# Kernel tuning notes

Measured on AMD Instinct MI355X. Metric: run time of the kernel, lower is better.

## Reference

```python
import jax, jax.numpy as jnp
import numpy as np

B, S, D = 8, 2048, 256


def setup_inputs() -> dict:
    key = jax.random.key(0)
    kq, kk, kv, km = jax.random.split(key, 4)
    q = jax.random.normal(kq, (B, S, D), dtype=jnp.float32)
    k = jax.random.normal(kk, (B, S, D), dtype=jnp.float32)
    v = jax.random.normal(kv, (B, S, D), dtype=jnp.float32)
    mask = jax.random.randint(km, (B, S, S), 0, 2, dtype=jnp.int32)
    return {"q": q, "k": k, "v": v, "mask": mask}


def reference(q, k, v, mask):
    d_k = q.shape[-1]
    scale = 1.0 / jnp.sqrt(jnp.float32(d_k))
    # scores: [B, S, S]
    attn = jnp.einsum('bqd,bkd->bqk', q, k) * scale
    attn = jnp.where(mask == 0, jnp.float32(-1e9), attn)
    attn = jax.nn.softmax(attn, axis=-1)
    out = jnp.einsum('bqk,bkd->bqd', attn, v)
    return (out, attn)
```

## Files before the change

kernel.cpp:

```cpp
#include <hip/hip_runtime.h>

constexpr int B = 8, S = 2048, D = 256;
constexpr int TQ = 32;
constexpr float SCALE = 0.0625f;
constexpr int PSTRIDE = 2056;

typedef __attribute__((ext_vector_type(8))) short bf16x8;
typedef __attribute__((ext_vector_type(4))) float f32x4;

__device__ __forceinline__ short f2bf(float f) {
    union { float f; unsigned u; } c; c.f = f;
    unsigned u = c.u + 0x7fffu + ((c.u >> 16) & 1u);
    return (short)(u >> 16);
}

__global__ __launch_bounds__(256) void prepass(
    const float* __restrict__ k, const float* __restrict__ v,
    short* __restrict__ kb, short* __restrict__ vtb)
{
    __shared__ float tile[64][65];
    const int blk = blockIdx.x;
    const int tid = threadIdx.x;

    if (blk < 4096) {
        int i = blk * 256 + tid;
        float4 x = ((const float4*)k)[i];
        short4 o; o.x = f2bf(x.x); o.y = f2bf(x.y); o.z = f2bf(x.z); o.w = f2bf(x.w);
        ((short4*)kb)[i] = o;
    } else {
        int blk2 = blk - 4096;
        int b = blk2 >> 7, rem = blk2 & 127;
        int d0 = (rem & 3) * 64, k0 = (rem >> 2) * 64;
        int tr = tid >> 4, tc = tid & 15;
        const float* vb = v + (size_t)b * S * D;
        #pragma unroll
        for (int r = 0; r < 4; ++r) {
            int key = r * 16 + tr;
            float4 x = *(const float4*)(vb + (size_t)(k0 + key) * D + d0 + tc * 4);
            tile[key][tc * 4 + 0] = x.x; tile[key][tc * 4 + 1] = x.y;
            tile[key][tc * 4 + 2] = x.z; tile[key][tc * 4 + 3] = x.w;
        }
        __syncthreads();
        short* vtbb = vtb + (size_t)b * D * S;
        #pragma unroll
        for (int r = 0; r < 4; ++r) {
            int d = r * 16 + tr;
            short4 o;
            o.x = f2bf(tile[tc * 4 + 0][d]); o.y = f2bf(tile[tc * 4 + 1][d]);
            o.z = f2bf(tile[tc * 4 + 2][d]); o.w = f2bf(tile[tc * 4 + 3][d]);
            *(short4*)(vtbb + (size_t)(d0 + d) * S + k0 + tc * 4) = o;
        }
    }
}

__global__ __launch_bounds__(512, 2) void attn_mfma(
    const float* __restrict__ qf, const short* __restrict__ kb,
    const short* __restrict__ vtb, const int* __restrict__ maskg,
    float* __restrict__ outg, float* __restrict__ attng)
{
    const int b = blockIdx.x & 7;
    const int i0 = (blockIdx.x >> 3) * TQ;
    const int tid = threadIdx.x;
    const int wave = tid >> 6, lane = tid & 63;
    const int quad = lane >> 4, l16 = lane & 15;

    __shared__ short p_lds[TQ][PSTRIDE];
    __shared__ float red[8][TQ];

    unsigned long long mb[2];
    #pragma unroll
    for (int mt = 0; mt < 2; ++mt) {
        const int* mrow = maskg + ((size_t)b * S + i0 + mt * 16 + l16) * S + wave * 256 + quad * 4;
        unsigned long long bits = 0;
        #pragma unroll
        for (int c = 0; c < 2; ++c) {
            int4 t[8];
            #pragma unroll
            for (int j = 0; j < 8; ++j)
                t[j] = *(const int4*)(mrow + (c * 8 + j) * 16);
            #pragma unroll
            for (int j = 0; j < 8; ++j) {
                const int nt = c * 8 + j;
                unsigned long long nib = (t[j].x != 0 ? 1ull : 0ull)
                                       | (t[j].y != 0 ? 2ull : 0ull)
                                       | (t[j].z != 0 ? 4ull : 0ull)
                                       | (t[j].w != 0 ? 8ull : 0ull);
                bits |= nib << (nt * 4);
            }
        }
        mb[mt] = bits;
    }

    bf16x8 aq[2][8];
    const float* qbase = qf + ((size_t)b * S + i0) * D;
    #pragma unroll
    for (int mt = 0; mt < 2; ++mt)
        #pragma unroll
        for (int ks = 0; ks < 8; ++ks) {
            const float* p = qbase + (size_t)(mt * 16 + l16) * D + ks * 32 + quad * 8;
            float4 x0 = *(const float4*)p;
            float4 x1 = *(const float4*)(p + 4);
            bf16x8 a;
            a[0] = f2bf(x0.x); a[1] = f2bf(x0.y); a[2] = f2bf(x0.z); a[3] = f2bf(x0.w);
            a[4] = f2bf(x1.x); a[5] = f2bf(x1.y); a[6] = f2bf(x1.z); a[7] = f2bf(x1.w);
            aq[mt][ks] = a;
        }

    f32x4 acc[2][16];
    #pragma unroll
    for (int mt = 0; mt < 2; ++mt)
        #pragma unroll
        for (int nt = 0; nt < 16; ++nt)
            acc[mt][nt] = f32x4{0.f, 0.f, 0.f, 0.f};

    const short* kbase = kb + (size_t)b * S * D;
    #pragma unroll
    for (int nt = 0; nt < 16; ++nt) {
        const int n0 = wave * 256 + nt * 16;
        bf16x8 bk[8];
        #pragma unroll
        for (int ks = 0; ks < 8; ++ks)
            bk[ks] = *(const bf16x8*)(kbase + (size_t)(n0 + l16) * D + ks * 32 + quad * 8);
        #pragma unroll
        for (int ks = 0; ks < 8; ++ks) {
            acc[0][nt] = __builtin_amdgcn_mfma_f32_16x16x32_bf16(bk[ks], aq[0][ks], acc[0][nt], 0, 0, 0);
            acc[1][nt] = __builtin_amdgcn_mfma_f32_16x16x32_bf16(bk[ks], aq[1][ks], acc[1][nt], 0, 0, 0);
        }
    }

    float rsum[2] = {0.f, 0.f};
    #pragma unroll
    for (int mt = 0; mt < 2; ++mt) {
        #pragma unroll
        for (int nt = 0; nt < 16; ++nt) {
            #pragma unroll
            for (int r = 0; r < 4; ++r) {
                float e = ((mb[mt] >> (nt * 4 + r)) & 1ull)
                        ? __expf(acc[mt][nt][r] * SCALE) : 0.0f;
                acc[mt][nt][r] = e;
                rsum[mt] += e;
            }
        }
    }
    #pragma unroll
    for (int mt = 0; mt < 2; ++mt) {
        float v = rsum[mt];
        v += __shfl_xor(v, 16); v += __shfl_xor(v, 32);
        if (quad == 0) red[wave][mt * 16 + l16] = v;
    }
    __syncthreads();

    float inv[2];
    #pragma unroll
    for (int mt = 0; mt < 2; ++mt) {
        float tot = 0.f;
        #pragma unroll
        for (int w = 0; w < 8; ++w) tot += red[w][mt * 16 + l16];
        inv[mt] = 1.0f / tot;
    }

    #pragma unroll
    for (int mt = 0; mt < 2; ++mt) {
        float* arow = attng + ((size_t)b * S + i0 + mt * 16 + l16) * S + wave * 256 + quad * 4;
        #pragma unroll
        for (int nt = 0; nt < 16; ++nt) {
            float4 p4; short4 pb;
            float p0 = acc[mt][nt][0] * inv[mt];
            float p1 = acc[mt][nt][1] * inv[mt];
            float p2 = acc[mt][nt][2] * inv[mt];
            float p3 = acc[mt][nt][3] * inv[mt];
            p4.x = p0; p4.y = p1; p4.z = p2; p4.w = p3;
            pb.x = f2bf(p0); pb.y = f2bf(p1); pb.z = f2bf(p2); pb.w = f2bf(p3);
            *(float4*)(arow + nt * 16) = p4;
            *(short4*)&p_lds[mt * 16 + l16][wave * 256 + nt * 16 + quad * 4] = pb;
        }
    }
    __syncthreads();

    f32x4 oacc[2][2];
    #pragma unroll
    for (int mt = 0; mt < 2; ++mt)
        #pragma unroll
        for (int nc = 0; nc < 2; ++nc) oacc[mt][nc] = f32x4{0.f, 0.f, 0.f, 0.f};

    const short* vbase = vtb + (size_t)b * D * S;
    const int nb = wave * 32;
    for (int ks = 0; ks < 64; ++ks) {
        bf16x8 ap[2], bv[2];
        #pragma unroll
        for (int mt = 0; mt < 2; ++mt)
            ap[mt] = *(const bf16x8*)&p_lds[mt * 16 + l16][ks * 32 + quad * 8];
        #pragma unroll
        for (int nc = 0; nc < 2; ++nc)
            bv[nc] = *(const bf16x8*)(vbase + (size_t)(nb + nc * 16 + l16) * S + ks * 32 + quad * 8);
        #pragma unroll
        for (int mt = 0; mt < 2; ++mt)
            #pragma unroll
            for (int nc = 0; nc < 2; ++nc)
                oacc[mt][nc] = __builtin_amdgcn_mfma_f32_16x16x32_bf16(ap[mt], bv[nc], oacc[mt][nc], 0, 0, 0);
    }

    #pragma unroll
    for (int mt = 0; mt < 2; ++mt)
        #pragma unroll
        for (int nc = 0; nc < 2; ++nc)
            #pragma unroll
            for (int r = 0; r < 4; ++r) {
                int row = i0 + mt * 16 + quad * 4 + r;
                int col = nb + nc * 16 + l16;
                outg[((size_t)b * S + row) * D + col] = oacc[mt][nc][r];
            }
}

extern "C" void kernel_launch(void* const* d_in, const int* in_sizes, int n_in,
                              void* d_out, int out_size, void* d_ws, size_t ws_size,
                              hipStream_t stream) {
    const float* q    = (const float*)d_in[0];
    const float* k    = (const float*)d_in[1];
    const float* v    = (const float*)d_in[2];
    const int*   mask = (const int*)d_in[3];
    float* out  = (float*)d_out;
    float* attn = out + (size_t)B * S * D;

    const size_t N = (size_t)B * S * D;
    short* kb  = (short*)d_ws;
    short* vtb = kb + N;

    prepass<<<dim3(5120), 256, 0, stream>>>(k, v, kb, vtb);
    attn_mfma<<<dim3((S / TQ) * B), 512, 0, stream>>>(q, kb, vtb, mask, out, attn);
}
```

Before: 409.5 us.

## Interleave mask loads and softmax exp with QK^T MFMA loop, lighten barrier

```diff
diff --git a/kernel.cpp b/kernel.cpp
--- a/kernel.cpp
+++ b/kernel.cpp
@@ -67,30 +67,6 @@
     __shared__ short p_lds[TQ][PSTRIDE];
     __shared__ float red[8][TQ];
 
-    unsigned long long mb[2];
-    #pragma unroll
-    for (int mt = 0; mt < 2; ++mt) {
-        const int* mrow = maskg + ((size_t)b * S + i0 + mt * 16 + l16) * S + wave * 256 + quad * 4;
-        unsigned long long bits = 0;
-        #pragma unroll
-        for (int c = 0; c < 2; ++c) {
-            int4 t[8];
-            #pragma unroll
-            for (int j = 0; j < 8; ++j)
-                t[j] = *(const int4*)(mrow + (c * 8 + j) * 16);
-            #pragma unroll
-            for (int j = 0; j < 8; ++j) {
-                const int nt = c * 8 + j;
-                unsigned long long nib = (t[j].x != 0 ? 1ull : 0ull)
-                                       | (t[j].y != 0 ? 2ull : 0ull)
-                                       | (t[j].z != 0 ? 4ull : 0ull)
-                                       | (t[j].w != 0 ? 8ull : 0ull);
-                bits |= nib << (nt * 4);
-            }
-        }
-        mb[mt] = bits;
-    }
-
     bf16x8 aq[2][8];
     const float* qbase = qf + ((size_t)b * S + i0) * D;
     #pragma unroll
@@ -113,10 +89,16 @@
         for (int nt = 0; nt < 16; ++nt)
             acc[mt][nt] = f32x4{0.f, 0.f, 0.f, 0.f};
 
+    float rsum[2] = {0.f, 0.f};
     const short* kbase = kb + (size_t)b * S * D;
+    const int* mbase0 = maskg + ((size_t)b * S + i0 + l16) * S + wave * 256 + quad * 4;
+    const int* mbase1 = mbase0 + (size_t)16 * S;
+
     #pragma unroll
     for (int nt = 0; nt < 16; ++nt) {
         const int n0 = wave * 256 + nt * 16;
+        int4 m0 = *(const int4*)(mbase0 + nt * 16);
+        int4 m1 = *(const int4*)(mbase1 + nt * 16);
         bf16x8 bk[8];
         #pragma unroll
         for (int ks = 0; ks < 8; ++ks)
@@ -126,22 +108,17 @@
             acc[0][nt] = __builtin_amdgcn_mfma_f32_16x16x32_bf16(bk[ks], aq[0][ks], acc[0][nt], 0, 0, 0);
             acc[1][nt] = __builtin_amdgcn_mfma_f32_16x16x32_bf16(bk[ks], aq[1][ks], acc[1][nt], 0, 0, 0);
         }
-    }
-
-    float rsum[2] = {0.f, 0.f};
-    #pragma unroll
-    for (int mt = 0; mt < 2; ++mt) {
-        #pragma unroll
-        for (int nt = 0; nt < 16; ++nt) {
-            #pragma unroll
-            for (int r = 0; r < 4; ++r) {
-                float e = ((mb[mt] >> (nt * 4 + r)) & 1ull)
-                        ? __expf(acc[mt][nt][r] * SCALE) : 0.0f;
-                acc[mt][nt][r] = e;
-                rsum[mt] += e;
-            }
-        }
-    }
+        const int mm0[4] = {m0.x, m0.y, m0.z, m0.w};
+        const int mm1[4] = {m1.x, m1.y, m1.z, m1.w};
+        #pragma unroll
+        for (int r = 0; r < 4; ++r) {
+            float e0 = mm0[r] ? __expf(acc[0][nt][r] * SCALE) : 0.0f;
+            acc[0][nt][r] = e0; rsum[0] += e0;
+            float e1 = mm1[r] ? __expf(acc[1][nt][r] * SCALE) : 0.0f;
+            acc[1][nt][r] = e1; rsum[1] += e1;
+        }
+    }
+
     #pragma unroll
     for (int mt = 0; mt < 2; ++mt) {
         float v = rsum[mt];
@@ -175,7 +152,10 @@
             *(short4*)&p_lds[mt * 16 + l16][wave * 256 + nt * 16 + quad * 4] = pb;
         }
     }
-    __syncthreads();
+
+    asm volatile("s_waitcnt lgkmcnt(0)" ::: "memory");
+    __builtin_amdgcn_s_barrier();
+    asm volatile("" ::: "memory");
 
     f32x4 oacc[2][2];
     #pragma unroll
```

New measurement: 412.6 us. About the same (+0.7%).
